# Kernel tuning notes

Measured on AMD Instinct MI355X. Metric: run time of the kernel, lower is better.

Reference implementation:

```python
import jax, jax.numpy as jnp
import numpy as np

B = 256          # batch
T = 256          # block_size (tril mask requires seq_len == 256)
E = 384          # n_embed
H = 6            # n_head
HS = E // H      # head_size = 64
EPS = 1e-5       # torch LayerNorm default


def layernorm(x, g, b):
    m = x.mean(-1, keepdims=True)
    v = x.var(-1, keepdims=True)  # population variance, matches torch LN
    return (x - m) * jax.lax.rsqrt(v + EPS) * g + b


def setup_inputs() -> dict:
    key = jax.random.key(0)
    ks = jax.random.split(key, 8)
    s = lambda i, shape: jax.random.normal(ks[i], shape, jnp.float32) * 0.02
    return {
        "x": jax.random.normal(ks[0], (B, T, E), jnp.float32),
        # per-head Q/K/V linears (bias=False) packed along output dim: [E, H*HS]
        "Wq": s(1, (E, E)), "Wk": s(2, (E, E)), "Wv": s(3, (E, E)),
        "Wo": s(4, (E, E)), "bo": jnp.zeros((E,), jnp.float32),
        "W1": s(5, (E, 4 * E)), "b1": jnp.zeros((4 * E,), jnp.float32),
        "W2": s(6, (4 * E, E)), "b2": jnp.zeros((E,), jnp.float32),
        "g1": jnp.ones((E,), jnp.float32), "be1": jnp.zeros((E,), jnp.float32),
        "g2": jnp.ones((E,), jnp.float32), "be2": jnp.zeros((E,), jnp.float32),
    }


def reference(x, Wq, Wk, Wv, Wo, bo, W1, b1, W2, b2, g1, be1, g2, be2):
    # Block.forward: ffwd(ln2(sa(ln1(x)) + x)) + x   (dropout = identity at eval)
    h = layernorm(x, g1, be1)                                  # [B,T,E]
    q = (h @ Wq).reshape(B, T, H, HS)
    k = (h @ Wk).reshape(B, T, H, HS)
    v = (h @ Wv).reshape(B, T, H, HS)
    wei = jnp.einsum('bqhd,bkhd->bhqk', q, k) * (HS ** -0.5)   # [B,H,T,T]
    mask = jnp.tril(jnp.ones((T, T), dtype=bool))
    wei = jnp.where(mask, wei, -jnp.inf)
    wei = jax.nn.softmax(wei, axis=-1)
    attn = jnp.einsum('bhqk,bkhd->bqhd', wei, v).reshape(B, T, E)
    sa = attn @ Wo + bo                                        # output projection
    y = sa + x                                                 # residual 1
    h2 = layernorm(y, g2, be2)
    ff = jax.nn.relu(h2 @ W1 + b1) @ W2 + b2                   # FFN
    return ff + x                                              # residual 2 (to x!)
```

## Files before the change

### kernel.cpp

```cpp
#include <hip/hip_runtime.h>
#include <hip/hip_bf16.h>

typedef unsigned short bfu;
typedef __attribute__((ext_vector_type(8))) short short8;
typedef __attribute__((ext_vector_type(4))) float f32x4;

__device__ __forceinline__ bfu f2bf(float f) {
  return __builtin_bit_cast(bfu, __float2bfloat16(f));
}

__device__ __forceinline__ void gld16(const void* g, void* l) {
  __builtin_amdgcn_global_load_lds(
      (const __attribute__((address_space(1))) void*)g,
      (__attribute__((address_space(3))) void*)l, 16, 0, 0);
}

__device__ __forceinline__ int swz8(int row, int sl) {
  return (row << 7) + (((sl ^ (row & 7)) & 7) << 4);
}

__device__ __forceinline__ int swz(int row, int slot) {
  const int unit = row >> 1;
  const int s8 = ((row & 1) << 2) | slot;
  return (unit << 7) + (((s8 ^ unit) & 7) << 4) + ((s8 >> 3) << 7);
}
__device__ __forceinline__ void unswz(int p, int& row, int& colel) {
  const int unit = p >> 7;
  const int s8 = ((p >> 4) & 7) ^ (unit & 7);
  row = (unit << 1) | (s8 >> 2);
  colel = (s8 & 3) << 3;
}

__global__ void transpose_all(const float* __restrict__ Wq, const float* __restrict__ Wk,
                              const float* __restrict__ Wv, const float* __restrict__ Wo,
                              const float* __restrict__ W1, const float* __restrict__ W2,
                              bfu* __restrict__ wqkvT, bfu* __restrict__ woT,
                              bfu* __restrict__ w1T, bfu* __restrict__ w2T) {
  int idx = blockIdx.x * 256 + threadIdx.x;
  if (idx < 4 * 147456) {
    int r = idx / 147456, i = idx - r * 147456;
    int k = i / 384, n = i - k * 384;
    const float* W = r == 0 ? Wq : r == 1 ? Wk : r == 2 ? Wv : Wo;
    bfu* dst = r < 3 ? wqkvT + r * 147456 : woT;
    dst[n * 384 + k] = f2bf(W[i]);
  } else if (idx < 4 * 147456 + 589824) {
    int i = idx - 4 * 147456;
    int k = i / 1536, n = i - k * 1536;
    w1T[n * 384 + k] = f2bf(W1[i]);
  } else if (idx < 4 * 147456 + 2 * 589824) {
    int i = idx - 4 * 147456 - 589824;
    int k = i / 384, n = i - k * 384;
    w2T[(size_t)n * 1536 + k] = f2bf(W2[i]);
  }
}

__launch_bounds__(256)
__global__ void ln_kernel(const float* __restrict__ in, const float* __restrict__ g,
                          const float* __restrict__ be, bfu* __restrict__ out) {
  const int wv = threadIdx.x >> 6, ln = threadIdx.x & 63;
  const size_t row = (size_t)blockIdx.x * 4 + wv;
  const float* p = in + row * 384;
  float v[6], s = 0.f, ss = 0.f;
#pragma unroll
  for (int i = 0; i < 6; i++) { v[i] = p[i * 64 + ln]; s += v[i]; ss += v[i] * v[i]; }
#pragma unroll
  for (int m = 1; m < 64; m <<= 1) { s += __shfl_xor(s, m); ss += __shfl_xor(ss, m); }
  const float mean = s * (1.f / 384.f);
  const float rs = rsqrtf(ss * (1.f / 384.f) - mean * mean + 1e-5f);
  bfu* q = out + row * 384;
#pragma unroll
  for (int i = 0; i < 6; i++) {
    const int c = i * 64 + ln;
    q[c] = f2bf((v[i] - mean) * rs * g[c] + be[c]);
  }
}

template <int BIAS, int RELU, int RES, int OUTBF>
__launch_bounds__(512)
__global__ void gemm3b(const bfu* __restrict__ A, const bfu* __restrict__ Bt,
                       const float* __restrict__ bias, const float* __restrict__ res,
                       void* __restrict__ Cout, int N, int K, int ntn) {
  __shared__ char sm[3 * 49152];
  const int tid = threadIdx.x;
  const int wv = tid >> 6, ln = tid & 63;
  const int cpx = gridDim.x >> 3;
  const int wg = (blockIdx.x & 7) * cpx + (blockIdx.x >> 3);
  const int bm = wg / ntn, bn = wg - bm * ntn;
  const int m0 = bm << 8, n0 = bn << 7;
  const int wr = wv >> 2, wc = wv & 3;
  const int fr = ln & 15, fslot = ln >> 4;
  const int lr = ln >> 3, lsl = (ln & 7) ^ lr;

  f32x4 acc[8][2];
#pragma unroll
  for (int i = 0; i < 8; i++)
#pragma unroll
    for (int j = 0; j < 2; j++) acc[i][j] = f32x4{0.f, 0.f, 0.f, 0.f};

  auto stageA = [&](int dbuf, int kt, int half) {
    char* smA = sm + dbuf * 49152;
    const int col = (kt << 6) + (lsl << 3);
#pragma unroll
    for (int i = 0; i < 2; ++i) {
      const int c = (wv << 2) + (half << 1) + i;
      gld16(A + (size_t)(m0 + (c << 3) + lr) * K + col, smA + (c << 10));
    }
  };
  auto stageB = [&](int dbuf, int kt, int j) {
    char* smB = sm + dbuf * 49152 + 32768;
    const int col = (kt << 6) + (lsl << 3);
    const int c = (wv << 1) + j;
    gld16(Bt + (size_t)(n0 + (c << 3) + lr) * K + col, smB + (c << 10));
  };

  const int nk = K >> 6;
  stageA(0, 0, 0); stageA(0, 0, 1); stageB(0, 0, 0); stageB(0, 0, 1);
  stageA(1, 1, 0); stageA(1, 1, 1); stageB(1, 1, 0); stageB(1, 1, 1);
  asm volatile("s_waitcnt vmcnt(6)" ::: "memory");
  __builtin_amdgcn_s_barrier();

  int cb = 0;
  for (int k = 0; k < nk; ++k) {
    const char* smA = sm + cb * 49152;
    const char* smB = smA + 32768;
    int sb = cb + 2; if (sb >= 3) sb -= 3;
    const bool st = (k + 2) < nk;
#pragma unroll
    for (int mh = 0; mh < 2; ++mh) {
      short8 af[4][2];
#pragma unroll
      for (int i = 0; i < 4; ++i)
#pragma unroll
        for (int ks = 0; ks < 2; ++ks)
          af[i][ks] = *(const short8*)(smA +
              swz8(wr * 128 + mh * 64 + i * 16 + fr, ks * 4 + fslot));
#pragma unroll
      for (int nh = 0; nh < 2; ++nh) {
        short8 bf[2];
#pragma unroll
        for (int ks = 0; ks < 2; ++ks)
          bf[ks] = *(const short8*)(smB + swz8(wc * 32 + nh * 16 + fr, ks * 4 + fslot));
        if (st) {
          if (mh == 0 && nh == 0) stageA(sb, k + 2, 0);
          if (mh == 0 && nh == 1) stageA(sb, k + 2, 1);
          if (mh == 1 && nh == 0) stageB(sb, k + 2, 0);
          if (mh == 1 && nh == 1) stageB(sb, k + 2, 1);
        }
        __builtin_amdgcn_s_barrier();
        asm volatile("s_waitcnt lgkmcnt(0)" ::: "memory");
        __builtin_amdgcn_sched_barrier(0);
        __builtin_amdgcn_s_setprio(1);
#pragma unroll
        for (int i = 0; i < 4; ++i)
#pragma unroll
          for (int ks = 0; ks < 2; ++ks)
            acc[mh * 4 + i][nh] = __builtin_amdgcn_mfma_f32_16x16x32_bf16(
                af[i][ks], bf[ks], acc[mh * 4 + i][nh], 0, 0, 0);
        __builtin_amdgcn_s_setprio(0);
        if (mh == 1 && nh == 1 && k + 1 < nk) {
          if (st) asm volatile("s_waitcnt vmcnt(6)" ::: "memory");
          else    asm volatile("s_waitcnt vmcnt(0)" ::: "memory");
        }
        __builtin_amdgcn_s_barrier();
      }
    }
    cb = (cb + 1 == 3) ? 0 : cb + 1;
  }

  const int rq = (ln >> 4) << 2;
#pragma unroll
  for (int mi = 0; mi < 8; mi++) {
#pragma unroll
    for (int ni = 0; ni < 2; ni++) {
      const int row = m0 + wr * 128 + mi * 16 + rq;
      const int col = n0 + wc * 32 + ni * 16 + fr;
      float bv = 0.f;
      if (BIAS) bv = bias[col];
#pragma unroll
      for (int r = 0; r < 4; r++) {
        float v = acc[mi][ni][r] + bv;
        if (RELU) v = fmaxf(v, 0.f);
        const size_t idx = (size_t)(row + r) * N + col;
        if (RES) v += res[idx];
        if (OUTBF) ((bfu*)Cout)[idx] = f2bf(v);
        else       ((float*)Cout)[idx] = v;
      }
    }
  }
}

__launch_bounds__(512)
__global__ void row_gemm(const bfu* __restrict__ A, const bfu* __restrict__ Bt,
                         const float* __restrict__ bias, const float* __restrict__ res,
                         const float* __restrict__ g, const float* __restrict__ be,
                         void* __restrict__ Cout, int K) {
  __shared__ bfu a_sm[4][128 * 32];
  __shared__ bfu b_sm[4][384 * 32];
  __shared__ float lnp[4][128][2];
  const int tid = threadIdx.x;
  const int wv = tid >> 6, ln = tid & 63;
  const int wr = wv >> 2, wc = wv & 3;
  const int fr = ln & 15, fslot = ln >> 4;
  const int m0 = blockIdx.x << 7;

  f32x4 acc[4][6];
#pragma unroll
  for (int i = 0; i < 4; i++)
#pragma unroll
    for (int j = 0; j < 6; j++) acc[i][j] = f32x4{0.f, 0.f, 0.f, 0.f};

  auto stage = [&](int buf, int kt) {
#pragma unroll
    for (int i = 0; i < 4; ++i) {
      const int c = wv * 4 + i;
      const int cc = (c < 8) ? c : (c - 8);
      const int p = cc * 1024 + (ln << 4);
      int r, colel;
      unswz(p, r, colel);
      const int col = kt * 32 + colel;
      if (c < 8)
        gld16(A + (size_t)(m0 + r) * K + col, (char*)a_sm[buf] + cc * 1024);
      else
        gld16(Bt + (size_t)r * K + col, (char*)b_sm[buf] + cc * 1024);
    }
  };

  const int nk = K >> 5;
#pragma unroll
  for (int i = 0; i < 3; ++i)
    if (i < nk) stage(i, i);

  for (int kt = 0; kt < nk; ++kt) {
    const int rem = nk - 1 - kt;
    if (rem >= 2)      asm volatile("s_waitcnt vmcnt(8)" ::: "memory");
    else if (rem == 1) asm volatile("s_waitcnt vmcnt(4)" ::: "memory");
    else               asm volatile("s_waitcnt vmcnt(0)" ::: "memory");
    __builtin_amdgcn_s_barrier();
    __builtin_amdgcn_sched_barrier(0);
    if (kt + 3 < nk) stage((kt + 3) & 3, kt + 3);
    const int cb = kt & 3;
    short8 af[4], bfr[6];
#pragma unroll
    for (int mi = 0; mi < 4; mi++)
      af[mi] = *(const short8*)((const char*)a_sm[cb] + swz(wr * 64 + mi * 16 + fr, fslot));
#pragma unroll
    for (int ni = 0; ni < 6; ni++)
      bfr[ni] = *(const short8*)((const char*)b_sm[cb] + swz(wc * 96 + ni * 16 + fr, fslot));
    __builtin_amdgcn_s_setprio(1);
#pragma unroll
    for (int mi = 0; mi < 4; mi++)
#pragma unroll
      for (int ni = 0; ni < 6; ni++)
        acc[mi][ni] = __builtin_amdgcn_mfma_f32_16x16x32_bf16(af[mi], bfr[ni], acc[mi][ni], 0, 0, 0);
    __builtin_amdgcn_s_setprio(0);
  }

  const int rq = (ln >> 4) << 2;
#pragma unroll
  for (int mi = 0; mi < 4; mi++) {
    const int row = wr * 64 + mi * 16 + rq;
#pragma unroll
    for (int ni = 0; ni < 6; ni++) {
      const int col = wc * 96 + ni * 16 + fr;
      const float bv = bias[col];
#pragma unroll
      for (int r = 0; r < 4; r++)
        acc[mi][ni][r] += bv + res[(size_t)(m0 + row + r) * 384 + col];
    }
  }

#pragma unroll
  for (int mi = 0; mi < 4; mi++) {
    float s[4] = {0.f, 0.f, 0.f, 0.f}, ss[4] = {0.f, 0.f, 0.f, 0.f};
#pragma unroll
    for (int ni = 0; ni < 6; ni++)
#pragma unroll
      for (int r = 0; r < 4; r++) {
        const float v = acc[mi][ni][r];
        s[r] += v; ss[r] += v * v;
      }
#pragma unroll
    for (int m = 1; m < 16; m <<= 1)
#pragma unroll
      for (int r = 0; r < 4; r++) {
        s[r] += __shfl_xor(s[r], m);
        ss[r] += __shfl_xor(ss[r], m);
      }
    if (fr == 0) {
#pragma unroll
      for (int r = 0; r < 4; r++) {
        lnp[wc][wr * 64 + mi * 16 + rq + r][0] = s[r];
        lnp[wc][wr * 64 + mi * 16 + rq + r][1] = ss[r];
      }
    }
  }
  __syncthreads();
#pragma unroll
  for (int mi = 0; mi < 4; mi++) {
#pragma unroll
    for (int r = 0; r < 4; r++) {
      const int row = wr * 64 + mi * 16 + rq + r;
      const float sm = lnp[0][row][0] + lnp[1][row][0] + lnp[2][row][0] + lnp[3][row][0];
      const float sq = lnp[0][row][1] + lnp[1][row][1] + lnp[2][row][1] + lnp[3][row][1];
      const float mean = sm * (1.f / 384.f);
      const float rs = rsqrtf(sq * (1.f / 384.f) - mean * mean + 1e-5f);
#pragma unroll
      for (int ni = 0; ni < 6; ni++) {
        const int col = wc * 96 + ni * 16 + fr;
        ((bfu*)Cout)[(size_t)(m0 + row) * 384 + col] =
            f2bf((acc[mi][ni][r] - mean) * rs * g[col] + be[col]);
      }
    }
  }
}

#define KPAD 72
#define VPAD 264
#define PPAD 264

__launch_bounds__(512)
__global__ void attn_kernel(const bfu* __restrict__ qkv, bfu* __restrict__ ob) {
  __shared__ bfu k_sm[256 * KPAD];
  __shared__ bfu vt_sm[64 * VPAD];
  __shared__ bfu p_sm[8 * 16 * PPAD];
  const int b = blockIdx.x / 6, h = blockIdx.x - b * 6;
  const int tid = threadIdx.x;
  const int wv = tid >> 6, ln = tid & 63;
  const int fr = ln & 15, fc = (ln >> 4) << 3;
  const size_t inbase = (size_t)b * 256 * 1152 + h * 64;
  const bfu* qb = qkv + inbase;
  const bfu* kb = qkv + inbase + 384;
  const bfu* vb = qkv + inbase + 768;
  const size_t obase = (size_t)b * 256 * 384 + h * 64;

  {
    const int row = tid >> 1;
    const int dh = (tid & 1) << 5;
    const bfu* kg = kb + (size_t)row * 1152 + dh;
    const bfu* vg = vb + (size_t)row * 1152 + dh;
#pragma unroll
    for (int i = 0; i < 4; i++) {
      short8 t8 = *(const short8*)(kg + i * 8);
      *(short8*)&k_sm[row * KPAD + dh + i * 8] = t8;
      short8 v8 = *(const short8*)(vg + i * 8);
#pragma unroll
      for (int j = 0; j < 8; j++)
        vt_sm[(dh + i * 8 + j) * VPAD + row] = (bfu)v8[j];
    }
  }
  __syncthreads();

  bfu* pw = &p_sm[wv * 16 * PPAD];
  const int rq = (ln >> 4) << 2;

#pragma unroll
  for (int si = 0; si < 2; ++si) {
    const int s = si ? (15 - wv) : wv;
    const int qr0 = s << 4;
    const int nf = s + 1;
    short8 aq[2];
#pragma unroll
    for (int dc = 0; dc < 2; dc++)
      aq[dc] = *(const short8*)(qb + (size_t)(qr0 + fr) * 1152 + dc * 32 + fc);

    f32x4 sacc[16];
#pragma unroll
    for (int f = 0; f < 16; f++) sacc[f] = f32x4{0.f, 0.f, 0.f, 0.f};
#pragma unroll
    for (int f = 0; f < 16; f++) if (f < nf) {
#pragma unroll
      for (int dc = 0; dc < 2; dc++) {
        short8 kf = *(const short8*)&k_sm[(f * 16 + fr) * KPAD + dc * 32 + fc];
        sacc[f] = __builtin_amdgcn_mfma_f32_16x16x32_bf16(aq[dc], kf, sacc[f], 0, 0, 0);
      }
    }
    float mr[4] = {-3e38f, -3e38f, -3e38f, -3e38f};
#pragma unroll
    for (int f = 0; f < 16; f++) if (f < nf) {
#pragma unroll
      for (int r = 0; r < 4; r++) {
        float sv = sacc[f][r] * 0.125f;
        if (f * 16 + fr > qr0 + rq + r) sv = -3e38f;
        sacc[f][r] = sv;
        mr[r] = fmaxf(mr[r], sv);
      }
    }
#pragma unroll
    for (int msk = 1; msk < 16; msk <<= 1) {
#pragma unroll
      for (int r = 0; r < 4; r++) mr[r] = fmaxf(mr[r], __shfl_xor(mr[r], msk));
    }
    float ls[4] = {0.f, 0.f, 0.f, 0.f};
#pragma unroll
    for (int f = 0; f < 16; f++) if (f < nf) {
#pragma unroll
      for (int r = 0; r < 4; r++) {
        float p = __expf(sacc[f][r] - mr[r]);
        sacc[f][r] = p;
        ls[r] += p;
      }
    }
#pragma unroll
    for (int msk = 1; msk < 16; msk <<= 1) {
#pragma unroll
      for (int r = 0; r < 4; r++) ls[r] += __shfl_xor(ls[r], msk);
    }
#pragma unroll
    for (int f = 0; f < 16; f++) if (f < nf) {
#pragma unroll
      for (int r = 0; r < 4; r++)
        pw[(rq + r) * PPAD + f * 16 + fr] = f2bf(sacc[f][r]);
    }
    if (nf & 1) {
#pragma unroll
      for (int r = 0; r < 4; r++) pw[(rq + r) * PPAD + nf * 16 + fr] = 0;
    }
    f32x4 oc[4];
#pragma unroll
    for (int n = 0; n < 4; n++) oc[n] = f32x4{0.f, 0.f, 0.f, 0.f};
    const int kcs = (nf + 1) >> 1;
#pragma unroll
    for (int kc = 0; kc < 8; ++kc) if (kc < kcs) {
      short8 pa = *(const short8*)&pw[fr * PPAD + kc * 32 + fc];
#pragma unroll
      for (int n = 0; n < 4; n++) {
        short8 vf = *(const short8*)&vt_sm[(n * 16 + fr) * VPAD + kc * 32 + fc];
        oc[n] = __builtin_amdgcn_mfma_f32_16x16x32_bf16(pa, vf, oc[n], 0, 0, 0);
      }
    }
    float inv[4];
#pragma unroll
    for (int r = 0; r < 4; r++) inv[r] = 1.f / ls[r];
#pragma unroll
    for (int n = 0; n < 4; n++) {
#pragma unroll
      for (int r = 0; r < 4; r++)
        ob[obase + (size_t)(qr0 + rq + r) * 384 + n * 16 + fr] = f2bf(oc[n][r] * inv[r]);
    }
  }
}

extern "C" void kernel_launch(void* const* d_in, const int* in_sizes, int n_in,
                              void* d_out, int out_size, void* d_ws, size_t ws_size,
                              hipStream_t stream) {
  const float* x   = (const float*)d_in[0];
  const float* Wq  = (const float*)d_in[1];
  const float* Wk  = (const float*)d_in[2];
  const float* Wv  = (const float*)d_in[3];
  const float* Wo  = (const float*)d_in[4];
  const float* bo  = (const float*)d_in[5];
  const float* W1  = (const float*)d_in[6];
  const float* b1  = (const float*)d_in[7];
  const float* W2  = (const float*)d_in[8];
  const float* b2  = (const float*)d_in[9];
  const float* g1  = (const float*)d_in[10];
  const float* be1 = (const float*)d_in[11];
  const float* g2  = (const float*)d_in[12];
  const float* be2 = (const float*)d_in[13];
  float* out = (float*)d_out;
  char* ws = (char*)d_ws;

  bfu* wqkvT = (bfu*)(ws + 0);
  bfu* woT   = (bfu*)(ws + 884736);
  bfu* w1T   = (bfu*)(ws + 1179648);
  bfu* w2T   = (bfu*)(ws + 2359296);
  char* H    = ws + 3538944;
  char* BIG  = H + 50331648;
  bfu* hb    = (bfu*)BIG;
  bfu* qkvb  = (bfu*)(BIG + 50331648);
  bfu* attnb = (bfu*)BIG;
  bfu* h2b   = (bfu*)H;
  bfu* ab    = (bfu*)BIG;

  transpose_all<<<6912, 256, 0, stream>>>(Wq, Wk, Wv, Wo, W1, W2, wqkvT, woT, w1T, w2T);

  ln_kernel<<<16384, 256, 0, stream>>>(x, g1, be1, hb);

  gemm3b<0, 0, 0, 1><<<2304, 512, 0, stream>>>(hb, wqkvT, nullptr, nullptr, qkvb, 1152, 384, 9);

  attn_kernel<<<1536, 512, 0, stream>>>(qkvb, attnb);

  row_gemm<<<512, 512, 0, stream>>>(attnb, woT, bo, x, g2, be2, h2b, 384);

  gemm3b<1, 1, 0, 1><<<3072, 512, 0, stream>>>(h2b, w1T, b1, nullptr, ab, 1536, 384, 12);

  gemm3b<1, 0, 1, 0><<<768, 512, 0, stream>>>(ab, w2T, b2, x, out, 384, 1536, 3);
}
```

Measured before the change: 509.6 us.

## Run FFN GEMMs in FP8 e4m3 with a new FP8 MFMA kernel

Quantizes W1/W2, the LN2 output and the ReLU activation to FP8 e4m3, and adds an FP8 GEMM kernel built on 16x16x32 fp8 MFMA with a triple-buffered LDS pipeline for both FFN matmuls. This halves operand bytes and raises the matrix-core rate for the largest GEMMs. In exchange it gives up precision: e4m3 quantization of activations and of small weights (0.02 scale) may exceed the accuracy tolerance.

```diff
diff --git a/kernel.cpp b/kernel.cpp
--- a/kernel.cpp
+++ b/kernel.cpp
@@ -1,12 +1,18 @@
 #include <hip/hip_runtime.h>
 #include <hip/hip_bf16.h>
+#include <hip/hip_fp8.h>
 
 typedef unsigned short bfu;
+typedef unsigned char f8u;
 typedef __attribute__((ext_vector_type(8))) short short8;
 typedef __attribute__((ext_vector_type(4))) float f32x4;
 
 __device__ __forceinline__ bfu f2bf(float f) {
   return __builtin_bit_cast(bfu, __float2bfloat16(f));
+}
+__device__ __forceinline__ f8u f2f8(float f) {
+  __hip_fp8_e4m3 t(f);
+  return t.__x;
 }
 
 __device__ __forceinline__ void gld16(const void* g, void* l) {
@@ -35,7 +41,7 @@
                               const float* __restrict__ Wv, const float* __restrict__ Wo,
                               const float* __restrict__ W1, const float* __restrict__ W2,
                               bfu* __restrict__ wqkvT, bfu* __restrict__ woT,
-                              bfu* __restrict__ w1T, bfu* __restrict__ w2T) {
+                              f8u* __restrict__ w1T, f8u* __restrict__ w2T) {
   int idx = blockIdx.x * 256 + threadIdx.x;
   if (idx < 4 * 147456) {
     int r = idx / 147456, i = idx - r * 147456;
@@ -46,11 +52,11 @@
   } else if (idx < 4 * 147456 + 589824) {
     int i = idx - 4 * 147456;
     int k = i / 1536, n = i - k * 1536;
-    w1T[n * 384 + k] = f2bf(W1[i]);
+    w1T[n * 384 + k] = f2f8(W1[i]);
   } else if (idx < 4 * 147456 + 2 * 589824) {
     int i = idx - 4 * 147456 - 589824;
     int k = i / 384, n = i - k * 384;
-    w2T[(size_t)n * 1536 + k] = f2bf(W2[i]);
+    w2T[(size_t)n * 1536 + k] = f2f8(W2[i]);
   }
 }
 
@@ -189,11 +195,121 @@
   }
 }
 
+template <int BIAS, int RELU, int RES, int OUTF8>
+__launch_bounds__(512)
+__global__ void gemm3f8(const f8u* __restrict__ A, const f8u* __restrict__ Bt,
+                        const float* __restrict__ bias, const float* __restrict__ res,
+                        void* __restrict__ Cout, int N, int K, int ntn) {
+  __shared__ char sm[3 * 24576];
+  const int tid = threadIdx.x;
+  const int wv = tid >> 6, ln = tid & 63;
+  const int cpx = gridDim.x >> 3;
+  const int wg = (blockIdx.x & 7) * cpx + (blockIdx.x >> 3);
+  const int bm = wg / ntn, bn = wg - bm * ntn;
+  const int m0 = bm << 8, n0 = bn << 7;
+  const int wr = wv >> 2, wc = wv & 3;
+  const int fr = ln & 15, fslot = ln >> 4;
+
+  f32x4 acc[8][2];
+#pragma unroll
+  for (int i = 0; i < 8; i++)
+#pragma unroll
+    for (int j = 0; j < 2; j++) acc[i][j] = f32x4{0.f, 0.f, 0.f, 0.f};
+
+  auto stageA = [&](int dbuf, int kt, int half) {
+    char* smA = sm + dbuf * 24576;
+    const int c = (wv << 1) + half;
+    gld16(A + (size_t)(m0 + (c << 4) + (ln >> 2)) * K + (kt << 6) + ((ln & 3) << 4),
+          smA + (c << 10));
+  };
+  auto stageB = [&](int dbuf, int kt) {
+    char* smB = sm + dbuf * 24576 + 16384;
+    const int c = wv;
+    gld16(Bt + (size_t)(n0 + (c << 4) + (ln >> 2)) * K + (kt << 6) + ((ln & 3) << 4),
+          smB + (c << 10));
+  };
+
+  const int nk = K >> 6;
+  stageA(0, 0, 0); stageA(0, 0, 1); stageB(0, 0);
+  stageA(1, 1, 0); stageA(1, 1, 1); stageB(1, 1);
+  asm volatile("s_waitcnt vmcnt(3)" ::: "memory");
+  __builtin_amdgcn_s_barrier();
+
+  int cb = 0;
+  for (int k = 0; k < nk; ++k) {
+    const char* smA = sm + cb * 24576;
+    const char* smB = smA + 16384;
+    int sb = cb + 2; if (sb >= 3) sb -= 3;
+    const bool st = (k + 2) < nk;
+#pragma unroll
+    for (int mh = 0; mh < 2; ++mh) {
+      long af[4][2];
+#pragma unroll
+      for (int i = 0; i < 4; ++i)
+#pragma unroll
+        for (int ks = 0; ks < 2; ++ks)
+          af[i][ks] = *(const long*)(smA +
+              (wr * 128 + mh * 64 + i * 16 + fr) * 64 + ks * 32 + fslot * 8);
+#pragma unroll
+      for (int nh = 0; nh < 2; ++nh) {
+        long bf[2];
+#pragma unroll
+        for (int ks = 0; ks < 2; ++ks)
+          bf[ks] = *(const long*)(smB +
+              (wc * 32 + nh * 16 + fr) * 64 + ks * 32 + fslot * 8);
+        if (st) {
+          if (mh == 0 && nh == 0) stageA(sb, k + 2, 0);
+          if (mh == 0 && nh == 1) stageA(sb, k + 2, 1);
+          if (mh == 1 && nh == 0) stageB(sb, k + 2);
+        }
+        __builtin_amdgcn_s_barrier();
+        asm volatile("s_waitcnt lgkmcnt(0)" ::: "memory");
+        __builtin_amdgcn_sched_barrier(0);
+        __builtin_amdgcn_s_setprio(1);
+#pragma unroll
+        for (int i = 0; i < 4; ++i)
+#pragma unroll
+          for (int ks = 0; ks < 2; ++ks)
+            acc[mh * 4 + i][nh] = __builtin_amdgcn_mfma_f32_16x16x32_fp8_fp8(
+                af[i][ks], bf[ks], acc[mh * 4 + i][nh], 0, 0, 0);
+        __builtin_amdgcn_s_setprio(0);
+        if (mh == 1 && nh == 1 && k + 1 < nk) {
+          if (st) asm volatile("s_waitcnt vmcnt(3)" ::: "memory");
+          else    asm volatile("s_waitcnt vmcnt(0)" ::: "memory");
+        }
+        __builtin_amdgcn_s_barrier();
+      }
+    }
+    cb = (cb + 1 == 3) ? 0 : cb + 1;
+  }
+
+  const int rq = (ln >> 4) << 2;
+#pragma unroll
+  for (int mi = 0; mi < 8; mi++) {
+#pragma unroll
+    for (int ni = 0; ni < 2; ni++) {
+      const int row = m0 + wr * 128 + mi * 16 + rq;
+      const int col = n0 + wc * 32 + ni * 16 + fr;
+      float bv = 0.f;
+      if (BIAS) bv = bias[col];
+#pragma unroll
+      for (int r = 0; r < 4; r++) {
+        float v = acc[mi][ni][r] + bv;
+        if (RELU) v = fmaxf(v, 0.f);
+        const size_t idx = (size_t)(row + r) * N + col;
+        if (RES) v += res[idx];
+        if (OUTF8) ((f8u*)Cout)[idx] = f2f8(v);
+        else       ((float*)Cout)[idx] = v;
+      }
+    }
+  }
+}
+
 __launch_bounds__(512)
 __global__ void row_gemm(const bfu* __restrict__ A, const bfu* __restrict__ Bt,
                          const float* __restrict__ bias, const float* __restrict__ res,
                          const float* __restrict__ g, const float* __restrict__ be,
-                         void* __restrict__ Cout, int K) {
+                         f8u* __restrict__ Cout, int K) {
   __shared__ bfu a_sm[4][128 * 32];
   __shared__ bfu b_sm[4][384 * 32];
   __shared__ float lnp[4][128][2];
@@ -307,8 +423,8 @@
 #pragma unroll
       for (int ni = 0; ni < 6; ni++) {
         const int col = wc * 96 + ni * 16 + fr;
-        ((bfu*)Cout)[(size_t)(m0 + row) * 384 + col] =
-            f2bf((acc[mi][ni][r] - mean) * rs * g[col] + be[col]);
+        Cout[(size_t)(m0 + row) * 384 + col] =
+            f2f8((acc[mi][ni][r] - mean) * rs * g[col] + be[col]);
       }
     }
   }
@@ -462,15 +578,15 @@
 
   bfu* wqkvT = (bfu*)(ws + 0);
   bfu* woT   = (bfu*)(ws + 884736);
-  bfu* w1T   = (bfu*)(ws + 1179648);
-  bfu* w2T   = (bfu*)(ws + 2359296);
+  f8u* w1T   = (f8u*)(ws + 1179648);
+  f8u* w2T   = (f8u*)(ws + 2359296);
   char* H    = ws + 3538944;
   char* BIG  = H + 50331648;
   bfu* hb    = (bfu*)BIG;
   bfu* qkvb  = (bfu*)(BIG + 50331648);
   bfu* attnb = (bfu*)BIG;
-  bfu* h2b   = (bfu*)H;
-  bfu* ab    = (bfu*)BIG;
+  f8u* h2b   = (f8u*)H;
+  f8u* ab    = (f8u*)BIG;
 
   transpose_all<<<6912, 256, 0, stream>>>(Wq, Wk, Wv, Wo, W1, W2, wqkvT, woT, w1T, w2T);
 
@@ -482,7 +598,7 @@
 
   row_gemm<<<512, 512, 0, stream>>>(attnb, woT, bo, x, g2, be2, h2b, 384);
 
-  gemm3b<1, 1, 0, 1><<<3072, 512, 0, stream>>>(h2b, w1T, b1, nullptr, ab, 1536, 384, 12);
-
-  gemm3b<1, 0, 1, 0><<<768, 512, 0, stream>>>(ab, w2T, b2, x, out, 384, 1536, 3);
-}
+  gemm3f8<1, 1, 0, 1><<<3072, 512, 0, stream>>>(h2b, w1T, b1, nullptr, ab, 1536, 384, 12);
+
+  gemm3f8<1, 0, 1, 0><<<768, 512, 0, stream>>>(ab, w2T, b2, x, out, 384, 1536, 3);
+}
```

Result: slower. 700.6 us (+37.5%).

## Replace 256x128 K64 GEMM with smaller 128x128 K32 tile and coalesced epilogues

Applied to the files above, without the earlier changes.

Swaps the 256x128 GEMM, which used a triple-buffered K=64 stage and 144KB of LDS, for a 128x128 tile with a double-buffered K=32 stage in 32KB of LDS. Launch bounds now request 6 blocks per SM, so occupancy should rise and the grid is twice as large. Epilogues for both the GEMM and row_gemm now stage results through LDS so global stores are 16-byte vectorised and coalesced rather than scattered scalar writes. The cost is less data reuse per tile, more barriers per K step, and more blocks re-reading A and B.

```diff
diff --git a/kernel.cpp b/kernel.cpp
--- a/kernel.cpp
+++ b/kernel.cpp
@@ -13,10 +13,6 @@
   __builtin_amdgcn_global_load_lds(
       (const __attribute__((address_space(1))) void*)g,
       (__attribute__((address_space(3))) void*)l, 16, 0, 0);
-}
-
-__device__ __forceinline__ int swz8(int row, int sl) {
-  return (row << 7) + (((sl ^ (row & 7)) & 7) << 4);
 }
 
 __device__ __forceinline__ int swz(int row, int slot) {
@@ -76,114 +72,124 @@
 }
 
 template <int BIAS, int RELU, int RES, int OUTBF>
-__launch_bounds__(512)
-__global__ void gemm3b(const bfu* __restrict__ A, const bfu* __restrict__ Bt,
-                       const float* __restrict__ bias, const float* __restrict__ res,
-                       void* __restrict__ Cout, int N, int K, int ntn) {
-  __shared__ char sm[3 * 49152];
+__launch_bounds__(512, 6)
+__global__ void gemm_k32(const bfu* __restrict__ A, const bfu* __restrict__ Bt,
+                         const float* __restrict__ bias, const float* __restrict__ res,
+                         void* __restrict__ Cout, int N, int K, int ntn) {
+  __shared__ char sm[2][16384];
   const int tid = threadIdx.x;
   const int wv = tid >> 6, ln = tid & 63;
   const int cpx = gridDim.x >> 3;
   const int wg = (blockIdx.x & 7) * cpx + (blockIdx.x >> 3);
   const int bm = wg / ntn, bn = wg - bm * ntn;
-  const int m0 = bm << 8, n0 = bn << 7;
+  const int m0 = bm << 7, n0 = bn << 7;
   const int wr = wv >> 2, wc = wv & 3;
   const int fr = ln & 15, fslot = ln >> 4;
-  const int lr = ln >> 3, lsl = (ln & 7) ^ lr;
-
-  f32x4 acc[8][2];
-#pragma unroll
-  for (int i = 0; i < 8; i++)
+
+  f32x4 acc[4][2];
+#pragma unroll
+  for (int i = 0; i < 4; i++)
 #pragma unroll
     for (int j = 0; j < 2; j++) acc[i][j] = f32x4{0.f, 0.f, 0.f, 0.f};
 
-  auto stageA = [&](int dbuf, int kt, int half) {
-    char* smA = sm + dbuf * 49152;
-    const int col = (kt << 6) + (lsl << 3);
-#pragma unroll
-    for (int i = 0; i < 2; ++i) {
-      const int c = (wv << 2) + (half << 1) + i;
-      gld16(A + (size_t)(m0 + (c << 3) + lr) * K + col, smA + (c << 10));
-    }
+  auto stage = [&](int buf, int kt) {
+    const int p = wv * 1024 + (ln << 4);
+    int r, colel;
+    unswz(p, r, colel);
+    const int col = kt * 32 + colel;
+    gld16(A + (size_t)(m0 + r) * K + col, sm[buf] + wv * 1024);
+    gld16(Bt + (size_t)(n0 + r) * K + col, sm[buf] + 8192 + wv * 1024);
   };
-  auto stageB = [&](int dbuf, int kt, int j) {
-    char* smB = sm + dbuf * 49152 + 32768;
-    const int col = (kt << 6) + (lsl << 3);
-    const int c = (wv << 1) + j;
-    gld16(Bt + (size_t)(n0 + (c << 3) + lr) * K + col, smB + (c << 10));
-  };
-
-  const int nk = K >> 6;
-  stageA(0, 0, 0); stageA(0, 0, 1); stageB(0, 0, 0); stageB(0, 0, 1);
-  stageA(1, 1, 0); stageA(1, 1, 1); stageB(1, 1, 0); stageB(1, 1, 1);
-  asm volatile("s_waitcnt vmcnt(6)" ::: "memory");
+
+  const int nk = K >> 5;
+  stage(0, 0);
+  stage(1, 1);
+  asm volatile("s_waitcnt vmcnt(2)" ::: "memory");
   __builtin_amdgcn_s_barrier();
 
-  int cb = 0;
-  for (int k = 0; k < nk; ++k) {
-    const char* smA = sm + cb * 49152;
-    const char* smB = smA + 32768;
-    int sb = cb + 2; if (sb >= 3) sb -= 3;
-    const bool st = (k + 2) < nk;
-#pragma unroll
-    for (int mh = 0; mh < 2; ++mh) {
-      short8 af[4][2];
-#pragma unroll
-      for (int i = 0; i < 4; ++i)
-#pragma unroll
-        for (int ks = 0; ks < 2; ++ks)
-          af[i][ks] = *(const short8*)(smA +
-              swz8(wr * 128 + mh * 64 + i * 16 + fr, ks * 4 + fslot));
-#pragma unroll
-      for (int nh = 0; nh < 2; ++nh) {
-        short8 bf[2];
-#pragma unroll
-        for (int ks = 0; ks < 2; ++ks)
-          bf[ks] = *(const short8*)(smB + swz8(wc * 32 + nh * 16 + fr, ks * 4 + fslot));
-        if (st) {
-          if (mh == 0 && nh == 0) stageA(sb, k + 2, 0);
-          if (mh == 0 && nh == 1) stageA(sb, k + 2, 1);
-          if (mh == 1 && nh == 0) stageB(sb, k + 2, 0);
-          if (mh == 1 && nh == 1) stageB(sb, k + 2, 1);
+  for (int kt = 0; kt < nk; ++kt) {
+    const int c = kt & 1;
+    const char* smA = sm[c];
+    const char* smB = smA + 8192;
+    short8 af[4], bf[2];
+#pragma unroll
+    for (int i = 0; i < 4; ++i)
+      af[i] = *(const short8*)(smA + swz(wr * 64 + i * 16 + fr, fslot));
+#pragma unroll
+    for (int n = 0; n < 2; ++n)
+      bf[n] = *(const short8*)(smB + swz(wc * 32 + n * 16 + fr, fslot));
+    asm volatile("s_waitcnt lgkmcnt(0)" ::: "memory");
+    __builtin_amdgcn_s_barrier();
+    __builtin_amdgcn_sched_barrier(0);
+    if (kt + 2 < nk) stage(c, kt + 2);
+    __builtin_amdgcn_s_setprio(1);
+#pragma unroll
+    for (int i = 0; i < 4; ++i)
+#pragma unroll
+      for (int n = 0; n < 2; ++n)
+        acc[i][n] = __builtin_amdgcn_mfma_f32_16x16x32_bf16(af[i], bf[n], acc[i][n], 0, 0, 0);
+    __builtin_amdgcn_s_setprio(0);
+    if (kt + 1 < nk) {
+      if (kt + 2 < nk) asm volatile("s_waitcnt vmcnt(2)" ::: "memory");
+      else             asm volatile("s_waitcnt vmcnt(0)" ::: "memory");
+      __builtin_amdgcn_s_barrier();
+    }
+  }
+
+  __syncthreads();
+
+  const int rq = fslot << 2;
+  if (OUTBF) {
+    constexpr int SSTR = 40;
+    bfu* scr = (bfu*)((char*)sm + wv * (SSTR * 16 * 2));
+#pragma unroll
+    for (int mi = 0; mi < 4; mi++) {
+#pragma unroll
+      for (int ni = 0; ni < 2; ni++) {
+        const int col = n0 + wc * 32 + ni * 16 + fr;
+        float bv = 0.f;
+        if (BIAS) bv = bias[col];
+#pragma unroll
+        for (int r = 0; r < 4; r++) {
+          float v = acc[mi][ni][r] + bv;
+          if (RELU) v = fmaxf(v, 0.f);
+          scr[(rq + r) * SSTR + ni * 16 + fr] = f2bf(v);
         }
-        __builtin_amdgcn_s_barrier();
-        asm volatile("s_waitcnt lgkmcnt(0)" ::: "memory");
-        __builtin_amdgcn_sched_barrier(0);
-        __builtin_amdgcn_s_setprio(1);
-#pragma unroll
-        for (int i = 0; i < 4; ++i)
-#pragma unroll
-          for (int ks = 0; ks < 2; ++ks)
-            acc[mh * 4 + i][nh] = __builtin_amdgcn_mfma_f32_16x16x32_bf16(
-                af[i][ks], bf[ks], acc[mh * 4 + i][nh], 0, 0, 0);
-        __builtin_amdgcn_s_setprio(0);
-        if (mh == 1 && nh == 1 && k + 1 < nk) {
-          if (st) asm volatile("s_waitcnt vmcnt(6)" ::: "memory");
-          else    asm volatile("s_waitcnt vmcnt(0)" ::: "memory");
+      }
+      {
+        const int row = ln >> 2, c16 = ln & 3;
+        short8 v = *(const short8*)((const char*)scr + row * SSTR * 2 + c16 * 16);
+        const int grow = m0 + wr * 64 + mi * 16 + row;
+        const int gcol = n0 + wc * 32 + c16 * 8;
+        *(short8*)((bfu*)Cout + (size_t)grow * N + gcol) = v;
+      }
+    }
+  } else {
+    constexpr int SSTR = 36;
+    float* scr = (float*)((char*)sm + wv * (SSTR * 16 * 4));
+#pragma unroll
+    for (int mi = 0; mi < 4; mi++) {
+#pragma unroll
+      for (int ni = 0; ni < 2; ni++) {
+#pragma unroll
+        for (int r = 0; r < 4; r++)
+          scr[(rq + r) * SSTR + ni * 16 + fr] = acc[mi][ni][r];
+      }
+#pragma unroll
+      for (int f0 = 0; f0 < 2; ++f0) {
+        const int f = f0 * 64 + ln;
+        const int row = f >> 3, cf = (f & 7) * 4;
+        f32x4 v = *(const f32x4*)(scr + row * SSTR + cf);
+        const int grow = m0 + wr * 64 + mi * 16 + row;
+        const int gcol = n0 + wc * 32 + cf;
+        const size_t idx = (size_t)grow * N + gcol;
+        if (BIAS) v += *(const f32x4*)(bias + gcol);
+        if (RELU) {
+#pragma unroll
+          for (int e = 0; e < 4; e++) v[e] = fmaxf(v[e], 0.f);
         }
-        __builtin_amdgcn_s_barrier();
-      }
-    }
-    cb = (cb + 1 == 3) ? 0 : cb + 1;
-  }
-
-  const int rq = (ln >> 4) << 2;
-#pragma unroll
-  for (int mi = 0; mi < 8; mi++) {
-#pragma unroll
-    for (int ni = 0; ni < 2; ni++) {
-      const int row = m0 + wr * 128 + mi * 16 + rq;
-      const int col = n0 + wc * 32 + ni * 16 + fr;
-      float bv = 0.f;
-      if (BIAS) bv = bias[col];
-#pragma unroll
-      for (int r = 0; r < 4; r++) {
-        float v = acc[mi][ni][r] + bv;
-        if (RELU) v = fmaxf(v, 0.f);
-        const size_t idx = (size_t)(row + r) * N + col;
-        if (RES) v += res[idx];
-        if (OUTBF) ((bfu*)Cout)[idx] = f2bf(v);
-        else       ((float*)Cout)[idx] = v;
+        if (RES) v += *(const f32x4*)(res + idx);
+        *(f32x4*)((float*)Cout + idx) = v;
       }
     }
   }
@@ -295,6 +301,7 @@
     }
   }
   __syncthreads();
+  bfu* scr = &b_sm[0][0];
 #pragma unroll
   for (int mi = 0; mi < 4; mi++) {
 #pragma unroll
@@ -307,10 +314,17 @@
 #pragma unroll
       for (int ni = 0; ni < 6; ni++) {
         const int col = wc * 96 + ni * 16 + fr;
-        ((bfu*)Cout)[(size_t)(m0 + row) * 384 + col] =
-            f2bf((acc[mi][ni][r] - mean) * rs * g[col] + be[col]);
-      }
-    }
+        scr[row * 384 + col] = f2bf((acc[mi][ni][r] - mean) * rs * g[col] + be[col]);
+      }
+    }
+  }
+  __syncthreads();
+#pragma unroll
+  for (int i = 0; i < 12; ++i) {
+    const int c = i * 512 + tid;
+    const int row = c / 48, off = (c - row * 48) * 8;
+    *(short8*)((bfu*)Cout + (size_t)(m0 + row) * 384 + off) =
+        *(const short8*)(scr + row * 384 + off);
   }
 }
 
@@ -476,13 +490,13 @@
 
   ln_kernel<<<16384, 256, 0, stream>>>(x, g1, be1, hb);
 
-  gemm3b<0, 0, 0, 1><<<2304, 512, 0, stream>>>(hb, wqkvT, nullptr, nullptr, qkvb, 1152, 384, 9);
+  gemm_k32<0, 0, 0, 1><<<4608, 512, 0, stream>>>(hb, wqkvT, nullptr, nullptr, qkvb, 1152, 384, 9);
 
   attn_kernel<<<1536, 512, 0, stream>>>(qkvb, attnb);
 
   row_gemm<<<512, 512, 0, stream>>>(attnb, woT, bo, x, g2, be2, h2b, 384);
 
-  gemm3b<1, 1, 0, 1><<<3072, 512, 0, stream>>>(h2b, w1T, b1, nullptr, ab, 1536, 384, 12);
-
-  gemm3b<1, 0, 1, 0><<<768, 512, 0, stream>>>(ab, w2T, b2, x, out, 384, 1536, 3);
-}
+  gemm_k32<1, 1, 0, 1><<<6144, 512, 0, stream>>>(h2b, w1T, b1, nullptr, ab, 1536, 384, 12);
+
+  gemm_k32<1, 0, 1, 0><<<1536, 512, 0, stream>>>(ab, w2T, b2, x, out, 384, 1536, 3);
+}
```

Measured after the change: 487.9 us. 4.3% less time.
